# Optimization experiments

Measured on AMD Instinct MI355X. Metric: run time of the kernel, lower is better.

## Reference

```python
import jax, jax.numpy as jnp
import numpy as np

B, K, C, Q, NCLS = 16, 36, 2048, 1024, 16
LIN = 1024
DIN = 2 * C + 16 + Q  # 5136


def _linear_params(key, din, dout, scale=0.02):
    kw, kb = jax.random.split(key)
    W = jax.random.normal(kw, (din, dout), dtype=jnp.float32) * scale
    b = jax.random.normal(kb, (dout,), dtype=jnp.float32) * scale
    return W, b


def setup_inputs() -> dict:
    key = jax.random.key(0)
    ks = jax.random.split(key, 12)
    box_feats = jax.random.normal(ks[0], (B, K, C), dtype=jnp.float32)
    q_feats = jax.random.normal(ks[1], (B, Q), dtype=jnp.float32)
    # valid boxes: x2>x1, y2>y1 so areas are strictly positive (no div-by-zero)
    x1y1 = jax.random.uniform(ks[2], (B, K, 2), dtype=jnp.float32)
    wh = jax.random.uniform(ks[3], (B, K, 2), dtype=jnp.float32, minval=0.05, maxval=1.0)
    box_coords = jnp.concatenate([x1y1, x1y1 + wh, wh], axis=-1)  # [B,K,6]
    index = jax.random.randint(ks[4], (B,), 1, K + 1)  # ragged box counts in [1,K]
    wholefeat = jax.random.normal(ks[5], (B, C), dtype=jnp.float32)
    pooled = jax.random.normal(ks[6], (B, C), dtype=jnp.float32)
    W1, b1 = _linear_params(ks[7], DIN, LIN)
    W2, b2 = _linear_params(ks[8], LIN, LIN)
    W3, b3 = _linear_params(ks[9], LIN, LIN)
    Wf1, bf1 = _linear_params(ks[10], LIN, LIN // 2)
    Wf2, bf2 = _linear_params(ks[11], LIN // 2, NCLS)
    return {"wholefeat": wholefeat, "pooled": pooled, "box_feats": box_feats,
            "q_feats": q_feats, "box_coords": box_coords, "index": index,
            "W1": W1, "b1": b1, "W2": W2, "b2": b2, "W3": W3, "b3": b3,
            "Wf1": Wf1, "bf1": bf1, "Wf2": Wf2, "bf2": bf2}


def _rn_forward(box_feats, q_feats, box_coords, index,
                W1, b1, W2, b2, W3, b3, Wf1, bf1, Wf2, bf2):
    b_, k_, c_ = box_feats.shape
    # ragged -> padded + mask: pair (i,j) valid iff i < index[b] and j < index[b]
    valid = (jnp.arange(k_)[None, :] < index[:, None]).astype(box_feats.dtype)  # [B,K]
    pair_mask = valid[:, :, None] * valid[:, None, :]  # [B,K,K]

    # pairwise dot of region features
    dot = jnp.einsum('bid,bjd->bij', box_feats, box_feats)[..., None]  # [B,K,K,1]

    bc = box_coords  # [B,K,6]
    area = (bc[..., 2] - bc[..., 0]) * (bc[..., 3] - bc[..., 1])  # [B,K]
    lr = jnp.maximum(0.0, jnp.minimum(bc[:, :, None, 2], bc[:, None, :, 2])
                     - jnp.maximum(bc[:, :, None, 0], bc[:, None, :, 0]))
    ud = jnp.maximum(0.0, jnp.minimum(bc[:, :, None, 3], bc[:, None, :, 3])
                     - jnp.maximum(bc[:, :, None, 1], bc[:, None, :, 1]))
    overlap = lr * ud  # [B,K,K]
    area_i = area[:, :, None]
    area_j = area[:, None, :]
    iou = (overlap / (area_i + area_j - overlap))[..., None]
    o_ij = (overlap / area_i)[..., None]
    o_ji = (overlap / area_j)[..., None]

    b_ij = jnp.broadcast_to(bc[:, :, None, :], (b_, k_, k_, 6))
    b_ji = jnp.broadcast_to(bc[:, None, :, :], (b_, k_, k_, 6))
    o_i = jnp.broadcast_to(box_feats[:, :, None, :], (b_, k_, k_, c_))
    o_j = jnp.broadcast_to(box_feats[:, None, :, :], (b_, k_, k_, c_))
    qst = jnp.broadcast_to(q_feats[:, None, None, :], (b_, k_, k_, q_feats.shape[-1]))

    # [B,K,K,5136] = [o_i, o_j, qst, dot, b_ij, b_ji, iou, o_ij, o_ji]
    feat = jnp.concatenate([o_i, o_j, qst, dot, b_ij, b_ji, iou, o_ij, o_ji], axis=-1)

    h = jax.nn.relu(feat @ W1 + b1)
    h = jax.nn.relu(h @ W2 + b2)
    h = jax.nn.relu(h @ W3 + b3)  # [B,K,K,1024]

    # masked sum-pool over all valid (i,j) pairs
    g = jnp.einsum('bijh,bij->bh', h, pair_mask)  # [B,1024]

    out = jax.nn.relu(g @ Wf1 + bf1) @ Wf2 + bf2  # [B,Ncls]
    return out


def reference(wholefeat, pooled, box_feats, q_feats, box_coords, index,
              W1, b1, W2, b2, W3, b3, Wf1, bf1, Wf2, bf2):
    # wholefeat / pooled are unused by the original forward as well
    return _rn_forward(box_feats, q_feats, box_coords, index,
                       W1, b1, W2, b2, W3, b3, Wf1, bf1, Wf2, bf2)
```

## Files before the change

### kernel.cpp

```cpp
#include <hip/hip_runtime.h>
#include <stdint.h>

typedef unsigned short u16;
typedef __attribute__((ext_vector_type(8))) short short8;
typedef __attribute__((ext_vector_type(4))) float f32x4;

#define Bn 16
#define Kn 36
#define Cn 2048
#define Qn 1024
#define LINn 1024
#define NPp 1296
#define NPAIRn 20736
#define NBIn 576

__device__ __forceinline__ u16 f2bf(float f) {
  union { float f; unsigned int u; } v; v.f = f;
  unsigned int r = v.u + 0x7FFFu + ((v.u >> 16) & 1u);
  return (u16)(r >> 16);
}

__device__ __forceinline__ void llds16(const void* g, void* l) {
  __builtin_amdgcn_global_load_lds((const __attribute__((address_space(1))) void*)g,
                                   (__attribute__((address_space(3))) void*)l, 16, 0, 0);
}

__global__ void k_transpose_all(const float* __restrict__ W1, const float* __restrict__ W2,
                                const float* __restrict__ W3, u16* __restrict__ W1abT,
                                u16* __restrict__ W2T, u16* __restrict__ W3T) {
  __shared__ float tile[32][33];
  int z = blockIdx.z;
  const float* src; u16* dst; int ld_dst;
  if (z == 0)      { if (blockIdx.y >= 32) return; src = W2; dst = W2T; ld_dst = 1024; }
  else if (z == 1) { if (blockIdx.y >= 32) return; src = W3; dst = W3T; ld_dst = 1024; }
  else if (z == 2) { src = W1; dst = W1abT; ld_dst = 2048; }
  else             { src = W1 + (size_t)2048 * 1024; dst = W1abT + (size_t)1024 * 2048; ld_dst = 2048; }
  int n0 = blockIdx.x * 32, k0 = blockIdx.y * 32;
  int tx = threadIdx.x & 31, ty = threadIdx.x >> 5;
#pragma unroll
  for (int r = 0; r < 32; r += 8)
    tile[ty + r][tx] = src[(size_t)(k0 + ty + r) * 1024 + (n0 + tx)];
  __syncthreads();
#pragma unroll
  for (int r = 0; r < 32; r += 8)
    dst[(size_t)(n0 + ty + r) * ld_dst + (k0 + tx)] = f2bf(tile[tx][ty + r]);
}

__global__ void k_f2b(const float4* __restrict__ src, ushort4* __restrict__ dst, int n4) {
  int i = blockIdx.x * 256 + threadIdx.x;
  if (i < n4) {
    float4 v = src[i];
    ushort4 o;
    o.x = f2bf(v.x); o.y = f2bf(v.y); o.z = f2bf(v.z); o.w = f2bf(v.w);
    dst[i] = o;
  }
}

__global__ void k_build(const int* __restrict__ index, int* __restrict__ pairList,
                        int* __restrict__ batchC, int* __restrict__ cnt2) {
  __shared__ int offs[17];
  int tid = threadIdx.x;
  if (tid == 0) {
    int o = 0;
    for (int b = 0; b < Bn; ++b) { offs[b] = o; int v = index[b]; o += v * v; }
    offs[16] = o;
    cnt2[0] = o;
    cnt2[1] = (o + 127) & ~127;
  }
  __syncthreads();
  int total = offs[16];
  int totalPad = (total + 127) & ~127;
  for (int b = 0; b < Bn; ++b) {
    int v = index[b]; int n = v * v; int base = offs[b];
    for (int t = tid; t < n; t += 256) {
      int i = t / v, j = t - i * v;
      pairList[base + t] = b * NPp + i * Kn + j;
      batchC[base + t] = b;
    }
  }
  for (int t = total + tid; t < totalPad; t += 256) {
    pairList[t] = 0;
    batchC[t] = 0;
  }
}

__global__ void k_pcinit(const float* __restrict__ b1, float* __restrict__ Pc) {
  int n = blockIdx.x * 256 + threadIdx.x;
  float v = b1[n];
#pragma unroll
  for (int b = 0; b < Bn; ++b) Pc[b * LINn + n] = v;
}

__global__ void k_pconst(const float* __restrict__ q, const float* __restrict__ W1,
                         float* __restrict__ Pc) {
  __shared__ float qs[Bn][32];
  int n = blockIdx.x * 256 + threadIdx.x;
  int k0 = blockIdx.y * 32;
  const float* Wq = W1 + (size_t)(2 * Cn) * LINn;
  for (int t = threadIdx.x; t < Bn * 32; t += 256) {
    int b = t >> 5, k = t & 31;
    qs[b][k] = q[b * Qn + k0 + k];
  }
  __syncthreads();
  float acc[Bn];
#pragma unroll
  for (int b = 0; b < Bn; ++b) acc[b] = 0.f;
  for (int k = 0; k < 32; ++k) {
    float w = Wq[(size_t)(k0 + k) * LINn + n];
#pragma unroll
    for (int b = 0; b < Bn; ++b) acc[b] += qs[b][k] * w;
  }
#pragma unroll
  for (int b = 0; b < Bn; ++b) atomicAdd(&Pc[b * LINn + n], acc[b]);
}

__global__ void k_pairscalars(const float* __restrict__ bfm, const float* __restrict__ bc,
                              const int* __restrict__ pairList, const int* __restrict__ cnt2,
                              float* __restrict__ dotC, float* __restrict__ iouC,
                              float* __restrict__ oijC, float* __restrict__ ojiC) {
  int cnt = cnt2[0];
  int lane = threadIdx.x & 63;
  for (int m = blockIdx.x * 4 + (threadIdx.x >> 6); m < cnt; m += gridDim.x * 4) {
    int p = pairList[m];
    int b = p / NPp, rem = p - b * NPp, i = rem / Kn, j = rem - (rem / Kn) * Kn;
    const float4* Ai = (const float4*)(bfm + (size_t)(b * Kn + i) * Cn);
    const float4* Aj = (const float4*)(bfm + (size_t)(b * Kn + j) * Cn);
    float s = 0.f;
#pragma unroll
    for (int t = 0; t < Cn / 4 / 64; ++t) {
      float4 x = Ai[lane + t * 64], y = Aj[lane + t * 64];
      s += x.x * y.x + x.y * y.y + x.z * y.z + x.w * y.w;
    }
#pragma unroll
    for (int o = 32; o > 0; o >>= 1) s += __shfl_down(s, o);
    if (lane == 0) {
      const float* ci = bc + (size_t)(b * Kn + i) * 6;
      const float* cj = bc + (size_t)(b * Kn + j) * 6;
      float ai = (ci[2] - ci[0]) * (ci[3] - ci[1]);
      float aj = (cj[2] - cj[0]) * (cj[3] - cj[1]);
      float lr = fmaxf(0.f, fminf(ci[2], cj[2]) - fmaxf(ci[0], cj[0]));
      float ud = fmaxf(0.f, fminf(ci[3], cj[3]) - fmaxf(ci[1], cj[1]));
      float ov = lr * ud;
      dotC[m] = s;
      iouC[m] = ov / (ai + aj - ov);
      oijC[m] = ov / ai;
      ojiC[m] = ov / aj;
    }
  }
}

__global__ void k_padd(const float* __restrict__ P12s, const float* __restrict__ Pc,
                       const float* __restrict__ bc, const float* __restrict__ W1,
                       float* __restrict__ P12) {
  int bi = blockIdx.x;
  int b = bi / Kn;
  const float* c = bc + (size_t)bi * 6;
  const float* W = W1 + (size_t)(2 * Cn + Qn + 1) * LINn;
  const size_t SL = (size_t)640 * 2048;
#pragma unroll
  for (int it = 0; it < 8; ++it) {
    int cc = it * 256 + threadIdx.x;
    size_t idx = (size_t)bi * 2048 + cc;
    float s = P12s[idx] + P12s[SL + idx] + P12s[2 * SL + idx] + P12s[3 * SL + idx];
    int n = cc & 1023;
    int rbase = (cc < 1024) ? 0 : 6;
    float a = 0.f;
#pragma unroll
    for (int t = 0; t < 6; ++t) a += c[t] * W[(size_t)(rbase + t) * LINn + n];
    if (cc < 1024) a += Pc[b * LINn + n];
    P12[idx] = s + a;
  }
}

__global__ void k_h1(const float* __restrict__ P12,
                     const float* __restrict__ dotC, const float* __restrict__ iouC,
                     const float* __restrict__ oijC, const float* __restrict__ ojiC,
                     const int* __restrict__ pairList, const int* __restrict__ cnt2,
                     const float* __restrict__ W1, u16* __restrict__ H1) {
  int cnt = cnt2[0];
  int t = threadIdx.x;
  const float4* wd = (const float4*)(W1 + (size_t)(2 * Cn + Qn) * LINn);
  const float4* wu = (const float4*)(W1 + (size_t)(2 * Cn + Qn + 13) * LINn);
  const float4* wa = (const float4*)(W1 + (size_t)(2 * Cn + Qn + 14) * LINn);
  const float4* wb = (const float4*)(W1 + (size_t)(2 * Cn + Qn + 15) * LINn);
  float4 e1 = wd[t], e2 = wu[t], e3 = wa[t], e4 = wb[t];
  for (int m = blockIdx.x; m < cnt; m += gridDim.x) {
    int p = pairList[m];
    int b = p / NPp, rem = p - b * NPp, i = rem / Kn, j = rem - (rem / Kn) * Kn;
    float d = dotC[m], u = iouC[m], o1 = oijC[m], o2 = ojiC[m];
    const float4* p1 = (const float4*)(P12 + (size_t)(b * Kn + i) * 2048);
    const float4* p2 = (const float4*)(P12 + (size_t)(b * Kn + j) * 2048 + 1024);
    ushort4* outp = (ushort4*)(H1 + (size_t)m * 1024);
    float4 v1 = p1[t], v2 = p2[t];
    ushort4 o;
    o.x = f2bf(fmaxf(v1.x + v2.x + d * e1.x + u * e2.x + o1 * e3.x + o2 * e4.x, 0.f));
    o.y = f2bf(fmaxf(v1.y + v2.y + d * e1.y + u * e2.y + o1 * e3.y + o2 * e4.y, 0.f));
    o.z = f2bf(fmaxf(v1.z + v2.z + d * e1.z + u * e2.z + o1 * e3.z + o2 * e4.z, 0.f));
    o.w = f2bf(fmaxf(v1.w + v2.w + d * e1.w + u * e2.w + o1 * e3.w + o2 * e4.w, 0.f));
    outp[t] = o;
  }
}

template <int EPI>
__global__ void __launch_bounds__(256) k_gemm(
    const u16* __restrict__ A, const u16* __restrict__ BT,
    int N, int K, int KC, int Mvalid, const int* __restrict__ cnt2,
    float* __restrict__ Cf, int CfSlice, u16* __restrict__ Cb,
    const float* __restrict__ bias,
    const int* __restrict__ batchC, float* __restrict__ G) {
  __shared__ u16 Alds[2][128 * 64];
  __shared__ u16 Blds[2][64 * 64];
  __shared__ float Gpart[(EPI == 2) ? (Bn * 64) : 4];

  const int tid = threadIdx.x;
  const int wave = tid >> 6, lane = tid & 63;
  const int wm = (wave >> 1) * 64, wn = (wave & 1) * 32;

  int Mv = Mvalid;
  int m0, n0;
  if (EPI == 0) {
    m0 = blockIdx.x * 128;
    n0 = blockIdx.y * 64;
  } else {
    Mv = cnt2[0];
    int nMt = (Mv + 127) >> 7;
    int nact = nMt * 16;
    int id = blockIdx.x;
    if (id >= nact) return;
    int q = nact >> 3, r = nact & 7;
    int xcd = id & 7, rank = id >> 3;
    int wg = (xcd < r ? xcd * (q + 1) : r * (q + 1) + (xcd - r) * q) + rank;
    m0 = (wg >> 4) * 128;
    n0 = (wg & 15) * 64;
  }
  if (EPI == 2) {
    for (int t = tid; t < Bn * 64; t += 256) Gpart[t] = 0.f;
  }

  f32x4 zero = {0.f, 0.f, 0.f, 0.f};
  f32x4 acc[4][2];
#pragma unroll
  for (int x = 0; x < 4; ++x)
#pragma unroll
    for (int y = 0; y < 2; ++y) acc[x][y] = zero;

  const int srow = tid >> 3;
  const int sslot = ((tid & 7) ^ (srow & 7)) * 16;
  const size_t ldb = (size_t)K * 2;

  auto stage = [&](int buf, int k0) {
    char* aB = (char*)Alds[buf] + wave * 1024;
    char* bB = (char*)Blds[buf] + wave * 1024;
#pragma unroll
    for (int c = 0; c < 4; ++c) {
      int rg = m0 + c * 32 + srow; if (rg >= Mv) rg = Mv - 1;
      llds16((const char*)A + (size_t)rg * ldb + (size_t)k0 * 2 + sslot, aB + c * 4096);
    }
#pragma unroll
    for (int c = 0; c < 2; ++c) {
      int rg = n0 + c * 32 + srow;
      llds16((const char*)BT + (size_t)rg * ldb + (size_t)k0 * 2 + sslot, bB + c * 4096);
    }
  };

  auto compute = [&](int buf) {
    const char* Ab = (const char*)Alds[buf];
    const char* Bb = (const char*)Blds[buf];
    short8 af[2][4], bfr[2][2];
#pragma unroll
    for (int kk = 0; kk < 2; ++kk) {
#pragma unroll
      for (int f = 0; f < 4; ++f) {
        int rA = wm + f * 16 + (lane & 15);
        int sl = ((kk * 4 + (lane >> 4)) ^ (rA & 7)) * 16;
        af[kk][f] = *(const short8*)(Ab + (size_t)rA * 128 + sl);
      }
#pragma unroll
      for (int f = 0; f < 2; ++f) {
        int rB = wn + f * 16 + (lane & 15);
        int sl = ((kk * 4 + (lane >> 4)) ^ (rB & 7)) * 16;
        bfr[kk][f] = *(const short8*)(Bb + (size_t)rB * 128 + sl);
      }
    }
#pragma unroll
    for (int kk = 0; kk < 2; ++kk)
#pragma unroll
      for (int x = 0; x < 4; ++x)
#pragma unroll
        for (int y = 0; y < 2; ++y)
          acc[x][y] = __builtin_amdgcn_mfma_f32_16x16x32_bf16(af[kk][x], bfr[kk][y],
                                                              acc[x][y], 0, 0, 0);
  };

  const int kbeg = blockIdx.z * KC;
  const int nt = KC >> 6;
  stage(0, kbeg);
  for (int t = 0; t < nt; ++t) {
    if (t + 1 < nt) {
      stage((t + 1) & 1, kbeg + (t + 1) * 64);
      asm volatile("s_waitcnt vmcnt(6)" ::: "memory");
    } else {
      asm volatile("s_waitcnt vmcnt(0)" ::: "memory");
    }
    __builtin_amdgcn_s_barrier();
    compute(t & 1);
    __builtin_amdgcn_s_barrier();
  }

  if (EPI == 0) {
    float* Cs = Cf + (size_t)blockIdx.z * CfSlice;
#pragma unroll
    for (int x = 0; x < 4; ++x) {
      int rb = m0 + wm + x * 16 + (lane >> 4) * 4;
#pragma unroll
      for (int r = 0; r < 4; ++r) {
        int row = rb + r;
        if (row < Mv) {
#pragma unroll
          for (int y = 0; y < 2; ++y)
            Cs[(size_t)row * N + (n0 + wn + y * 16 + (lane & 15))] = acc[x][y][r];
        }
      }
    }
  } else if (EPI == 1) {
#pragma unroll
    for (int x = 0; x < 4; ++x) {
      int rb = m0 + wm + x * 16 + (lane >> 4) * 4;
#pragma unroll
      for (int r = 0; r < 4; ++r) {
        int row = rb + r;
#pragma unroll
        for (int y = 0; y < 2; ++y) {
          int col = n0 + wn + y * 16 + (lane & 15);
          Cb[(size_t)row * N + col] = f2bf(fmaxf(acc[x][y][r] + bias[col], 0.f));
        }
      }
    }
  } else {
    const int cnt = Mv;
#pragma unroll
    for (int x = 0; x < 4; ++x) {
      int rb = m0 + wm + x * 16 + (lane >> 4) * 4;
      int b0 = batchC[rb], b1 = batchC[rb + 1], b2 = batchC[rb + 2], b3 = batchC[rb + 3];
      float mk0 = (rb     < cnt) ? 1.f : 0.f;
      float mk1 = (rb + 1 < cnt) ? 1.f : 0.f;
      float mk2 = (rb + 2 < cnt) ? 1.f : 0.f;
      float mk3 = (rb + 3 < cnt) ? 1.f : 0.f;
#pragma unroll
      for (int y = 0; y < 2; ++y) {
        int coll = wn + y * 16 + (lane & 15);
        float bs = bias[n0 + coll];
        float s0 = mk0 * fmaxf(acc[x][y][0] + bs, 0.f);
        float s1 = mk1 * fmaxf(acc[x][y][1] + bs, 0.f);
        float s2 = mk2 * fmaxf(acc[x][y][2] + bs, 0.f);
        float s3 = mk3 * fmaxf(acc[x][y][3] + bs, 0.f);
        if (b0 == b3) {
          atomicAdd(&Gpart[b0 * 64 + coll], s0 + s1 + s2 + s3);
        } else {
          atomicAdd(&Gpart[b0 * 64 + coll], s0);
          atomicAdd(&Gpart[b1 * 64 + coll], s1);
          atomicAdd(&Gpart[b2 * 64 + coll], s2);
          atomicAdd(&Gpart[b3 * 64 + coll], s3);
        }
      }
    }
    __syncthreads();
    for (int t2 = tid; t2 < Bn * 64; t2 += 256) {
      float v = Gpart[t2];
      if (v != 0.f) atomicAdd(&G[(t2 >> 6) * LINn + n0 + (t2 & 63)], v);
    }
  }
}

__global__ void k_final1(const float* __restrict__ G, const float* __restrict__ Wf1,
                         float* __restrict__ S) {
  __shared__ float g[128];
  int b = blockIdx.x, kz = blockIdx.y, tid = threadIdx.x;
  if (tid < 128) g[tid] = G[b * 1024 + kz * 128 + tid];
  __syncthreads();
  float acc = 0.f;
  const float* W = Wf1 + (size_t)(kz * 128) * 512 + tid;
  for (int k = 0; k < 128; ++k) acc += g[k] * W[(size_t)k * 512];
  atomicAdd(&S[b * 512 + tid], acc);
}

__global__ void k_final2(const float* __restrict__ S, const float* __restrict__ bf1,
                         const float* __restrict__ Wf2, const float* __restrict__ bf2,
                         float* __restrict__ out) {
  __shared__ float mid[512];
  __shared__ float part[256];
  int b = blockIdx.x, tid = threadIdx.x;
  for (int t = tid; t < 512; t += 256) mid[t] = fmaxf(S[b * 512 + t] + bf1[t], 0.f);
  __syncthreads();
  int o = tid & 15, seg = tid >> 4;
  float s = 0.f;
#pragma unroll
  for (int t = 0; t < 32; ++t) {
    int j = seg * 32 + t;
    s += mid[j] * Wf2[j * 16 + o];
  }
  part[tid] = s;
  __syncthreads();
  if (tid < 16) {
    float v = bf2[tid];
#pragma unroll
    for (int sg = 0; sg < 16; ++sg) v += part[sg * 16 + tid];
    out[b * 16 + tid] = v;
  }
}

extern "C" void kernel_launch(void* const* d_in, const int* in_sizes, int n_in,
                              void* d_out, int out_size, void* d_ws, size_t ws_size,
                              hipStream_t stream) {
  const float* box_feats  = (const float*)d_in[2];
  const float* q_feats    = (const float*)d_in[3];
  const float* box_coords = (const float*)d_in[4];
  const int*   index      = (const int*)d_in[5];
  const float* W1  = (const float*)d_in[6];
  const float* b1  = (const float*)d_in[7];
  const float* W2  = (const float*)d_in[8];
  const float* b2  = (const float*)d_in[9];
  const float* W3  = (const float*)d_in[10];
  const float* b3  = (const float*)d_in[11];
  const float* Wf1 = (const float*)d_in[12];
  const float* bf1 = (const float*)d_in[13];
  const float* Wf2 = (const float*)d_in[14];
  const float* bf2 = (const float*)d_in[15];
  float* out = (float*)d_out;

  char* ws = (char*)d_ws;
  size_t off = 0;
  auto alloc = [&](size_t bytes) { void* p = ws + off; off += (bytes + 255) & ~(size_t)255; return p; };
  u16* W1abT = (u16*)alloc((size_t)2048 * 2048 * 2);
  u16* W2T   = (u16*)alloc((size_t)1024 * 1024 * 2);
  u16* W3T   = (u16*)alloc((size_t)1024 * 1024 * 2);
  u16* BFb   = (u16*)alloc((size_t)NBIn * Cn * 2);
  float* P12s = (float*)alloc((size_t)4 * 640 * 2048 * 4);
  float* P12  = (float*)alloc((size_t)NBIn * 2048 * 4);
  float* Pc   = (float*)alloc((size_t)Bn * LINn * 4);
  float* dotC = (float*)alloc((size_t)NPAIRn * 4);
  float* iouC = (float*)alloc((size_t)NPAIRn * 4);
  float* oijC = (float*)alloc((size_t)NPAIRn * 4);
  float* ojiC = (float*)alloc((size_t)NPAIRn * 4);
  int* pairList = (int*)alloc((size_t)NPAIRn * 4);
  int* batchC   = (int*)alloc((size_t)NPAIRn * 4);
  int* cnt2     = (int*)alloc(64);
  float* G  = (float*)alloc((size_t)Bn * LINn * 4);
  float* S  = (float*)alloc((size_t)Bn * 512 * 4);
  u16* H1 = (u16*)alloc((size_t)NPAIRn * 1024 * 2);
  u16* H2 = (u16*)alloc((size_t)NPAIRn * 1024 * 2);

  k_transpose_all<<<dim3(32, 64, 4), 256, 0, stream>>>(W1, W2, W3, W1abT, W2T, W3T);
  k_f2b<<<(NBIn * Cn / 4 + 255) / 256, 256, 0, stream>>>((const float4*)box_feats,
                                                         (ushort4*)BFb, NBIn * Cn / 4);
  k_build<<<1, 256, 0, stream>>>(index, pairList, batchC, cnt2);
  k_pcinit<<<4, 256, 0, stream>>>(b1, Pc);
  k_pconst<<<dim3(4, 32), 256, 0, stream>>>(q_feats, W1, Pc);
  k_pairscalars<<<648, 256, 0, stream>>>(box_feats, box_coords, pairList, cnt2,
                                         dotC, iouC, oijC, ojiC);
  k_gemm<0><<<dim3(5, 32, 4), 256, 0, stream>>>(BFb, W1abT, 2048, 2048, 512, NBIn, nullptr,
                                                P12s, 640 * 2048, nullptr, nullptr,
                                                nullptr, nullptr);
  k_padd<<<NBIn, 256, 0, stream>>>(P12s, Pc, box_coords, W1, P12);
  k_h1<<<2592, 256, 0, stream>>>(P12, dotC, iouC, oijC, ojiC, pairList, cnt2, W1, H1);
  hipMemsetAsync(G, 0, (size_t)Bn * LINn * 4, stream);
  hipMemsetAsync(S, 0, (size_t)Bn * 512 * 4, stream);
  k_gemm<1><<<dim3(2592, 1, 1), 256, 0, stream>>>(H1, W2T, 1024, 1024, 1024, 0, cnt2,
                                                  nullptr, 0, H2, b2, nullptr, nullptr);
  k_gemm<2><<<dim3(2592, 1, 1), 256, 0, stream>>>(H2, W3T, 1024, 1024, 1024, 0, cnt2,
                                                  nullptr, 0, nullptr, b3, batchC, G);
  k_final1<<<dim3(16, 8), 512, 0, stream>>>(G, Wf1, S);
  k_final2<<<16, 256, 0, stream>>>(S, bf1, Wf2, bf2, out);
}
```

Measured before the change: 152.6 us.

## Reduce split-K GEMM partials via atomics into pre-initialized P12; parallelize pair build

The split-K first-layer GEMM now atomically accumulates its partial sums straight into P12. P12 is pre-initialized with the bias, constant and coordinate terms by a new k_pinit kernel. This removes the four-slice partial buffer and the separate reduction pass that read it back. The pair-list build kernel also now runs one block per batch instead of a single block. The trade-off is float atomic contention and non-deterministic summation order.

Result: slower. 156.8 us (+2.7%).

```diff
diff --git a/kernel.cpp b/kernel.cpp
--- a/kernel.cpp
+++ b/kernel.cpp
@@ -60,27 +60,30 @@
                         int* __restrict__ batchC, int* __restrict__ cnt2) {
   __shared__ int offs[17];
   int tid = threadIdx.x;
+  int b = blockIdx.x;
   if (tid == 0) {
     int o = 0;
-    for (int b = 0; b < Bn; ++b) { offs[b] = o; int v = index[b]; o += v * v; }
+    for (int i = 0; i < Bn; ++i) { offs[i] = o; int v = index[i]; o += v * v; }
     offs[16] = o;
-    cnt2[0] = o;
-    cnt2[1] = (o + 127) & ~127;
-  }
-  __syncthreads();
-  int total = offs[16];
-  int totalPad = (total + 127) & ~127;
-  for (int b = 0; b < Bn; ++b) {
-    int v = index[b]; int n = v * v; int base = offs[b];
-    for (int t = tid; t < n; t += 256) {
-      int i = t / v, j = t - i * v;
-      pairList[base + t] = b * NPp + i * Kn + j;
-      batchC[base + t] = b;
-    }
-  }
-  for (int t = total + tid; t < totalPad; t += 256) {
-    pairList[t] = 0;
-    batchC[t] = 0;
+    if (b == 0) {
+      cnt2[0] = o;
+      cnt2[1] = (o + 127) & ~127;
+    }
+  }
+  __syncthreads();
+  int v = index[b]; int n = v * v; int base = offs[b];
+  for (int t = tid; t < n; t += 256) {
+    int i = t / v, j = t - i * v;
+    pairList[base + t] = b * NPp + i * Kn + j;
+    batchC[base + t] = b;
+  }
+  if (b == 0) {
+    int total = offs[16];
+    int totalPad = (total + 127) & ~127;
+    for (int t = total + tid; t < totalPad; t += 256) {
+      pairList[t] = 0;
+      batchC[t] = 0;
+    }
   }
 }
 
@@ -149,26 +152,22 @@
   }
 }
 
-__global__ void k_padd(const float* __restrict__ P12s, const float* __restrict__ Pc,
-                       const float* __restrict__ bc, const float* __restrict__ W1,
-                       float* __restrict__ P12) {
+__global__ void k_pinit(const float* __restrict__ Pc, const float* __restrict__ bc,
+                        const float* __restrict__ W1, float* __restrict__ P12) {
   int bi = blockIdx.x;
   int b = bi / Kn;
   const float* c = bc + (size_t)bi * 6;
   const float* W = W1 + (size_t)(2 * Cn + Qn + 1) * LINn;
-  const size_t SL = (size_t)640 * 2048;
 #pragma unroll
   for (int it = 0; it < 8; ++it) {
     int cc = it * 256 + threadIdx.x;
-    size_t idx = (size_t)bi * 2048 + cc;
-    float s = P12s[idx] + P12s[SL + idx] + P12s[2 * SL + idx] + P12s[3 * SL + idx];
     int n = cc & 1023;
     int rbase = (cc < 1024) ? 0 : 6;
     float a = 0.f;
 #pragma unroll
     for (int t = 0; t < 6; ++t) a += c[t] * W[(size_t)(rbase + t) * LINn + n];
     if (cc < 1024) a += Pc[b * LINn + n];
-    P12[idx] = s + a;
+    P12[(size_t)bi * 2048 + cc] = a;
   }
 }
 
@@ -205,7 +204,7 @@
 __global__ void __launch_bounds__(256) k_gemm(
     const u16* __restrict__ A, const u16* __restrict__ BT,
     int N, int K, int KC, int Mvalid, const int* __restrict__ cnt2,
-    float* __restrict__ Cf, int CfSlice, u16* __restrict__ Cb,
+    float* __restrict__ Cf, u16* __restrict__ Cb,
     const float* __restrict__ bias,
     const int* __restrict__ batchC, float* __restrict__ G) {
   __shared__ u16 Alds[2][128 * 64];
@@ -308,7 +307,6 @@
   }
 
   if (EPI == 0) {
-    float* Cs = Cf + (size_t)blockIdx.z * CfSlice;
 #pragma unroll
     for (int x = 0; x < 4; ++x) {
       int rb = m0 + wm + x * 16 + (lane >> 4) * 4;
@@ -318,7 +316,8 @@
         if (row < Mv) {
 #pragma unroll
           for (int y = 0; y < 2; ++y)
-            Cs[(size_t)row * N + (n0 + wn + y * 16 + (lane & 15))] = acc[x][y][r];
+            atomicAdd(&Cf[(size_t)row * N + (n0 + wn + y * 16 + (lane & 15))],
+                      acc[x][y][r]);
         }
       }
     }
@@ -435,8 +434,7 @@
   u16* W2T   = (u16*)alloc((size_t)1024 * 1024 * 2);
   u16* W3T   = (u16*)alloc((size_t)1024 * 1024 * 2);
   u16* BFb   = (u16*)alloc((size_t)NBIn * Cn * 2);
-  float* P12s = (float*)alloc((size_t)4 * 640 * 2048 * 4);
-  float* P12  = (float*)alloc((size_t)NBIn * 2048 * 4);
+  float* P12  = (float*)alloc((size_t)640 * 2048 * 4);
   float* Pc   = (float*)alloc((size_t)Bn * LINn * 4);
   float* dotC = (float*)alloc((size_t)NPAIRn * 4);
   float* iouC = (float*)alloc((size_t)NPAIRn * 4);
@@ -453,22 +451,21 @@
   k_transpose_all<<<dim3(32, 64, 4), 256, 0, stream>>>(W1, W2, W3, W1abT, W2T, W3T);
   k_f2b<<<(NBIn * Cn / 4 + 255) / 256, 256, 0, stream>>>((const float4*)box_feats,
                                                          (ushort4*)BFb, NBIn * Cn / 4);
-  k_build<<<1, 256, 0, stream>>>(index, pairList, batchC, cnt2);
+  k_build<<<16, 256, 0, stream>>>(index, pairList, batchC, cnt2);
+  hipMemsetAsync(G, 0, (size_t)Bn * LINn * 4, stream);
+  hipMemsetAsync(S, 0, (size_t)Bn * 512 * 4, stream);
   k_pcinit<<<4, 256, 0, stream>>>(b1, Pc);
   k_pconst<<<dim3(4, 32), 256, 0, stream>>>(q_feats, W1, Pc);
   k_pairscalars<<<648, 256, 0, stream>>>(box_feats, box_coords, pairList, cnt2,
                                          dotC, iouC, oijC, ojiC);
+  k_pinit<<<NBIn, 256, 0, stream>>>(Pc, box_coords, W1, P12);
   k_gemm<0><<<dim3(5, 32, 4), 256, 0, stream>>>(BFb, W1abT, 2048, 2048, 512, NBIn, nullptr,
-                                                P12s, 640 * 2048, nullptr, nullptr,
-                                                nullptr, nullptr);
-  k_padd<<<NBIn, 256, 0, stream>>>(P12s, Pc, box_coords, W1, P12);
+                                                P12, nullptr, nullptr, nullptr, nullptr);
   k_h1<<<2592, 256, 0, stream>>>(P12, dotC, iouC, oijC, ojiC, pairList, cnt2, W1, H1);
-  hipMemsetAsync(G, 0, (size_t)Bn * LINn * 4, stream);
-  hipMemsetAsync(S, 0, (size_t)Bn * 512 * 4, stream);
   k_gemm<1><<<dim3(2592, 1, 1), 256, 0, stream>>>(H1, W2T, 1024, 1024, 1024, 0, cnt2,
-                                                  nullptr, 0, H2, b2, nullptr, nullptr);
+                                                  nullptr, H2, b2, nullptr, nullptr);
   k_gemm<2><<<dim3(2592, 1, 1), 256, 0, stream>>>(H2, W3T, 1024, 1024, 1024, 0, cnt2,
-                                                  nullptr, 0, nullptr, b3, batchC, G);
+                                                  nullptr, nullptr, b3, batchC, G);
   k_final1<<<dim3(16, 8), 512, 0, stream>>>(G, Wf1, S);
   k_final2<<<16, 256, 0, stream>>>(S, bf1, Wf2, bf2, out);
 }
```
